# Kernel optimization log

Measured on AMD Instinct MI355X. Metric: run time of the kernel, lower is better.

Reference implementation:

```python
import jax, jax.numpy as jnp
import numpy as np

NUM_GRAPHS = 16
NODES_PER = 1024
D = 128
H = 2
KPOS = 20
E = 262144


def _ln(x, g, b):
    mu = jnp.mean(x, axis=-1, keepdims=True)
    var = jnp.mean((x - mu) ** 2, axis=-1, keepdims=True)
    return (x - mu) * jax.lax.rsqrt(var + 1e-5) * g + b


def setup_inputs() -> dict:
    key = jax.random.key(0)
    ks = jax.random.split(key, 12)
    N = NUM_GRAPHS * NODES_PER
    s = 0.02
    return {
        "x": jax.random.normal(ks[0], (N, D), jnp.float32),
        "pos_enc": jax.random.normal(ks[1], (N, KPOS), jnp.float32),
        "pe_w": jax.random.normal(ks[2], (D, KPOS), jnp.float32) * s,
        "pe_b": jnp.zeros((D,), jnp.float32),
        "in_w": jax.random.normal(ks[3], (3 * D, D), jnp.float32) * s,
        "in_b": jnp.zeros((3 * D,), jnp.float32),
        "out_w": jax.random.normal(ks[4], (D, D), jnp.float32) * s,
        "out_b": jnp.zeros((D,), jnp.float32),
        "ln1_g": jnp.ones((D,), jnp.float32),
        "ln1_b": jnp.zeros((D,), jnp.float32),
        "ln2_g": jnp.ones((D,), jnp.float32),
        "ln2_b": jnp.zeros((D,), jnp.float32),
        "ff1_w": jax.random.normal(ks[5], (4 * D, D), jnp.float32) * s,
        "ff1_b": jnp.zeros((4 * D,), jnp.float32),
        "ff2_w": jax.random.normal(ks[6], (D, 4 * D), jnp.float32) * s,
        "ff2_b": jnp.zeros((D,), jnp.float32),
        "edge_index": jax.random.randint(ks[7], (2, E), 0, N, dtype=jnp.int32),
        "batch": jnp.repeat(jnp.arange(NUM_GRAPHS, dtype=jnp.int32), NODES_PER),
    }


def reference(x, pos_enc, pe_w, pe_b, in_w, in_b, out_w, out_b,
              ln1_g, ln1_b, ln2_g, ln2_b, ff1_w, ff1_b, ff2_w, ff2_b,
              edge_index, batch):
    # pos_enc Linear + add, then per-graph transformer (graphs equal-sized -> batched)
    h = x + pos_enc @ pe_w.T + pe_b  # (N, D)
    h = h.reshape(NUM_GRAPHS, NODES_PER, D)  # (B, S, D)

    hd = D // H
    qkv = h @ in_w.T + in_b  # (B, S, 3D)
    q, k, v = jnp.split(qkv, 3, axis=-1)

    def heads(t):
        return t.reshape(NUM_GRAPHS, NODES_PER, H, hd).transpose(0, 2, 1, 3)

    q, k, v = heads(q), heads(k), heads(v)  # (B, H, S, hd)
    scores = jnp.einsum('bhqd,bhkd->bhqk', q, k) / jnp.float32(np.sqrt(hd))
    attn = jax.nn.softmax(scores, axis=-1)
    ctx = jnp.einsum('bhqk,bhkd->bhqd', attn, v)
    ctx = ctx.transpose(0, 2, 1, 3).reshape(NUM_GRAPHS, NODES_PER, D)
    sa = ctx @ out_w.T + out_b

    # post-norm (PyTorch TransformerEncoderLayer default, eval mode: no dropout)
    h = _ln(h + sa, ln1_g, ln1_b)
    ff = jax.nn.relu(h @ ff1_w.T + ff1_b) @ ff2_w.T + ff2_b
    h = _ln(h + ff, ln2_g, ln2_b)
    return h.reshape(-1, D)
```

## Files before the change

kernel.cpp:

```cpp
#include <hip/hip_runtime.h>

typedef unsigned short u16;

#define NGRAPH 16
#define SEQ    1024
#define DIM    128
#define NHEAD  2
#define HDIM   64
#define KPOS   20
#define NTOT   (NGRAPH*SEQ)
#define QKVD   (3*DIM)

__device__ __forceinline__ float bf2f(u16 u) {
    return __uint_as_float(((unsigned int)u) << 16);
}
__device__ __forceinline__ u16 f2bf(float f) {
    unsigned int u = __float_as_uint(f);
    u += 0x7fffu + ((u >> 16) & 1u);
    return (u16)(u >> 16);
}

template<int CTRL>
__device__ __forceinline__ float dpp_ror(float x) {
    return __int_as_float(__builtin_amdgcn_update_dpp(
        __float_as_int(x), __float_as_int(x), CTRL, 0xF, 0xF, true));
}
__device__ __forceinline__ float row16_max(float x) {
    x = fmaxf(x, dpp_ror<0x121>(x));
    x = fmaxf(x, dpp_ror<0x122>(x));
    x = fmaxf(x, dpp_ror<0x124>(x));
    x = fmaxf(x, dpp_ror<0x128>(x));
    return x;
}
__device__ __forceinline__ float row16_sum(float x) {
    x += dpp_ror<0x121>(x);
    x += dpp_ror<0x122>(x);
    x += dpp_ror<0x124>(x);
    x += dpp_ror<0x128>(x);
    return x;
}

__device__ __forceinline__ float ld1(const void* p, int fbf, size_t i) {
    return fbf ? bf2f(((const u16*)p)[i]) : ((const float*)p)[i];
}
__device__ __forceinline__ float4 ldw8(const void* W, int fbf, size_t i) {
    if (fbf) return *(const float4*)((const u16*)W + i);
    const float* q = (const float*)W + i;
    float4 a = *(const float4*)q, b = *(const float4*)(q + 4);
    float4 r;
    u16* d = (u16*)&r;
    d[0]=f2bf(a.x); d[1]=f2bf(a.y); d[2]=f2bf(a.z); d[3]=f2bf(a.w);
    d[4]=f2bf(b.x); d[5]=f2bf(b.y); d[6]=f2bf(b.z); d[7]=f2bf(b.w);
    return r;
}

typedef __attribute__((ext_vector_type(8))) short bf16x8;
typedef __attribute__((ext_vector_type(4))) float f32x4;

__device__ __forceinline__ void gload16(const u16* g, u16* l) {
    __builtin_amdgcn_global_load_lds(
        (const __attribute__((address_space(1))) unsigned int*)(g),
        (__attribute__((address_space(3))) unsigned int*)(l), 16, 0, 0);
}
#define VMCNT0() asm volatile("s_waitcnt vmcnt(0)" ::: "memory")

__device__ __forceinline__ int detect_bf16(const u16* x) {
    int ok = 1;
    for (int i = 0; i < 256; i += 2) {
        unsigned e = (x[i] >> 7) & 0xFF;
        if (e < 60u || e > 180u) ok = 0;
    }
    return ok;
}
__global__ void detect_kernel(const u16* __restrict__ x, int* __restrict__ flag) {
    if (threadIdx.x == 0 && blockIdx.x == 0) *flag = detect_bf16(x);
}

__global__ __launch_bounds__(256)
void wconv_kernel(const void* __restrict__ in_w, const void* __restrict__ out_w,
                  const void* __restrict__ ff1_w, const void* __restrict__ ff2_w,
                  const u16* __restrict__ x,
                  u16* __restrict__ wbf, int* __restrict__ flag) {
    __shared__ int fsh;
    if (threadIdx.x == 0) {
        int ok = detect_bf16(x);
        fsh = ok;
        if (blockIdx.x == 0) *flag = ok;
    }
    __syncthreads();
    int fbf = fsh;
    int i8 = (blockIdx.x * 256 + threadIdx.x) * 8;
    const void* src; int off;
    if      (i8 <  49152) { src = in_w;  off = i8; }
    else if (i8 <  65536) { src = out_w; off = i8 - 49152; }
    else if (i8 < 131072) { src = ff1_w; off = i8 - 65536; }
    else                  { src = ff2_w; off = i8 - 131072; }
    *(float4*)&wbf[i8] = ldw8(src, fbf, off);
}

__global__ __launch_bounds__(256)
void pe_kernel(const void* __restrict__ x, const void* __restrict__ pos,
               const void* __restrict__ pe_w, const void* __restrict__ pe_b,
               u16* __restrict__ h0, const int* __restrict__ flag) {
    int fbf = *flag;
    __shared__ float wsh[DIM][KPOS + 1];
    int t = threadIdx.x;
    for (int i = t; i < DIM * KPOS; i += 256)
        wsh[i / KPOS][i % KPOS] = ld1(pe_w, fbf, i);
    __syncthreads();
    int row = blockIdx.x * 2 + (t >> 7), d = t & 127;
    float acc = 0.f;
#pragma unroll
    for (int k = 0; k < KPOS; ++k)
        acc += ld1(pos, fbf, (size_t)row * KPOS + k) * wsh[d][k];
    int rs = fbf ? 128 : 256;
    h0[(size_t)row * rs + d] =
        f2bf(ld1(x, fbf, (size_t)row * DIM + d) + acc + ld1(pe_b, fbf, d));
}

template<int EPI, int NK>
__global__ __launch_bounds__(256)
void mgemm2_kernel(const u16* __restrict__ A, const u16* __restrict__ W,
                   const void* __restrict__ bias, const u16* __restrict__ resid,
                   const void* __restrict__ lng, const void* __restrict__ lnb,
                   void* __restrict__ outp, u16* __restrict__ vt,
                   int Mtot, int AstrIn,
                   int arow0, int orow0, const int* __restrict__ flag) {
    const int K  = NK * 128;
    const int NB = (NK > 1) ? 2 : 1;
    int fbf  = *flag;
    int rs   = fbf ? 128 : 256;
    int Astr = (AstrIn < 0) ? rs : AstrIn;
    __shared__ __align__(16) u16 Ash[NB][64][128];
    __shared__ __align__(16) u16 Wsh[NB][128][128];
    int t = threadIdx.x;
    int w = t >> 6, lane = t & 63, l16 = lane & 15, quad = lane >> 4;
    int n0 = blockIdx.x * 64;
    int m0 = blockIdx.y * 128;
    int xr = (l16 & 7) << 3;
    f32x4 acc[8] = {};

    auto stage = [&](int c, int b) {
        int kc = c * 128;
#pragma unroll
        for (int i = 0; i < 4; ++i) {
            int r = w * 4 + i * 16 + (lane >> 4);
            int s = (lane & 15) ^ (r & 7);
            gload16(&A[(size_t)(arow0 + n0 + r) * Astr + kc + s * 8],
                    &Ash[b][w * 4 + i * 16][0]);
        }
#pragma unroll
        for (int i = 0; i < 8; ++i) {
            int r = w * 4 + i * 16 + (lane >> 4);
            int s = (lane & 15) ^ (r & 7);
            gload16(&W[(size_t)(m0 + r) * K + kc + s * 8],
                    &Wsh[b][w * 4 + i * 16][0]);
        }
    };

    stage(0, 0);
#pragma unroll 1
    for (int c = 0; c < NK; ++c) {
        VMCNT0();
        __syncthreads();
        if (c + 1 < NK) stage(c + 1, (c + 1) & (NB - 1));
        int b = c & (NB - 1);
        __builtin_amdgcn_s_setprio(1);
#pragma unroll
        for (int kk = 0; kk < 4; ++kk) {
            bf16x8 af = *(const bf16x8*)&Ash[b][w * 16 + l16][(kk * 32 + quad * 8) ^ xr];
#pragma unroll
            for (int s = 0; s < 8; ++s) {
                bf16x8 bf = *(const bf16x8*)&Wsh[b][s * 16 + l16][(kk * 32 + quad * 8) ^ xr];
                acc[s] = __builtin_amdgcn_mfma_f32_16x16x32_bf16(af, bf, acc[s], 0, 0, 0);
            }
        }
        __builtin_amdgcn_s_setprio(0);
    }
    float bb[8];
#pragma unroll
    for (int s = 0; s < 8; ++s) bb[s] = ld1(bias, fbf, m0 + s * 16 + l16);
    float gg[8], be[8];
    if (EPI >= 2) {
#pragma unroll
        for (int s = 0; s < 8; ++s) {
            gg[s] = ld1(lng, fbf, s * 16 + l16);
            be[s] = ld1(lnb, fbf, s * 16 + l16);
        }
    }
#pragma unroll
    for (int r = 0; r < 4; ++r) {
        int lr = w * 16 + quad * 4 + r;
        float v[8];
#pragma unroll
        for (int s = 0; s < 8; ++s) {
            v[s] = acc[s][r] + bb[s];
            if (EPI == 1) v[s] = fmaxf(v[s], 0.f);
        }
        if (EPI <= 1) {
            if (EPI == 0 && vt != nullptr && m0 == 256) {
                int n = n0 + lr;
                int bg = n >> 10, nl = n & 1023;
#pragma unroll
                for (int s = 0; s < 8; ++s)
                    vt[((size_t)(bg * 128) + s * 16 + l16) * SEQ + nl] = f2bf(v[s]);
            } else {
                u16* o = (u16*)outp;
#pragma unroll
                for (int s = 0; s < 8; ++s)
                    o[(size_t)(n0 + lr) * Mtot + m0 + s * 16 + l16] = f2bf(v[s]);
            }
        } else {
            size_t rg = (size_t)(orow0 + n0 + lr);
#pragma unroll
            for (int s = 0; s < 8; ++s)
                v[s] += bf2f(resid[rg * rs + s * 16 + l16]);
            float sm = 0.f, sq = 0.f;
#pragma unroll
            for (int s = 0; s < 8; ++s) { sm += v[s]; sq += v[s] * v[s]; }
            sm = row16_sum(sm);
            sq = row16_sum(sq);
            float mu  = sm * (1.f / DIM);
            float var = fmaxf(sq * (1.f / DIM) - mu * mu, 0.f);
            float rsq = rsqrtf(var + 1e-5f);
            if (EPI == 2) {
                u16* o = (u16*)outp;
#pragma unroll
                for (int s = 0; s < 8; ++s)
                    o[rg * rs + s * 16 + l16] =
                        f2bf((v[s] - mu) * rsq * gg[s] + be[s]);
            } else {
                if (fbf) {
                    u16* o = (u16*)outp;
#pragma unroll
                    for (int s = 0; s < 8; ++s)
                        o[rg * 128 + s * 16 + l16] =
                            f2bf((v[s] - mu) * rsq * gg[s] + be[s]);
                } else {
                    float* o = (float*)outp;
#pragma unroll
                    for (int s = 0; s < 8; ++s)
                        o[rg * 128 + s * 16 + l16] =
                            (v[s] - mu) * rsq * gg[s] + be[s];
                }
            }
        }
    }
}

__global__ __launch_bounds__(256)
void attn2_kernel(const u16* __restrict__ qkv, const u16* __restrict__ vtp,
                  u16* __restrict__ ctx) {
    __shared__ __align__(16) u16 Qsh[64][72];
    __shared__ __align__(16) u16 Ksh[2][64][64];
    __shared__ __align__(16) u16 Vsh[2][64][64];
    __shared__ u16 Psh[64][72];
    int t    = threadIdx.x;
    int w    = t >> 6;
    int lane = t & 63;
    int l16  = lane & 15;
    int quad = lane >> 4;
    int xr   = (l16 & 7) << 3;
    int L = blockIdx.x;
    int ngh = gridDim.x >> 4;
    int qt, gh;
    if (ngh >= 8) {
        int g8 = L & 7; int rest = L >> 3;
        qt = rest & 15; gh = (rest >> 4) * 8 + g8;
    } else {
        qt = L & 15; gh = L >> 4;
    }
    int b = gh >> 1, h = gh & 1;

#pragma unroll
    for (int i = 0; i < 2; ++i) {
        int idx = t + i * 256;
        int r = idx >> 3, d8 = (idx & 7) * 8;
        size_t n = (size_t)b * SEQ + qt * 64 + r;
        float4 qv = *(const float4*)&qkv[n * QKVD + h * HDIM + d8];
        u16* qp = (u16*)&qv;
#pragma unroll
        for (int j = 0; j < 8; ++j) qp[j] = f2bf(bf2f(qp[j]) * 0.125f);
        *(float4*)&Qsh[r][d8] = qv;
    }

    const u16* kbase = qkv + (size_t)b * SEQ * QKVD + DIM + h * HDIM;
    const u16* vbase = vtp + (size_t)((b * 2 + h) * 64) * SEQ;

    auto stageKV = [&](int kt, int bf) {
#pragma unroll
        for (int i = 0; i < 2; ++i) {
            int r = w * 8 + i * 32 + (lane >> 3);
            int s = (lane & 7) ^ (r & 7);
            gload16(&kbase[(size_t)(kt * 64 + r) * QKVD + s * 8],
                    &Ksh[bf][w * 8 + i * 32][0]);
        }
#pragma unroll
        for (int i = 0; i < 2; ++i) {
            int r = w * 8 + i * 32 + (lane >> 3);
            int s = (lane & 7) ^ (r & 7);
            gload16(&vbase[(size_t)r * SEQ + kt * 64 + s * 8],
                    &Vsh[bf][w * 8 + i * 32][0]);
        }
    };

    stageKV(0, 0);
    VMCNT0();
    __syncthreads();
    bf16x8 qa0 = *(const bf16x8*)&Qsh[w * 16 + l16][quad * 8];
    bf16x8 qa1 = *(const bf16x8*)&Qsh[w * 16 + l16][32 + quad * 8];

    f32x4 o[4] = {};
    float mrow[4] = {-1e30f, -1e30f, -1e30f, -1e30f};
    float lrow[4] = {};

#pragma unroll 1
    for (int kt = 0; kt < SEQ / 64; ++kt) {
        int cur = kt & 1;
        if (kt + 1 < SEQ / 64) stageKV(kt + 1, cur ^ 1);

        float sc[4][4];
        __builtin_amdgcn_s_setprio(1);
#pragma unroll
        for (int c = 0; c < 4; ++c) {
            bf16x8 kb0 = *(const bf16x8*)&Ksh[cur][c * 16 + l16][(quad * 8) ^ xr];
            bf16x8 kb1 = *(const bf16x8*)&Ksh[cur][c * 16 + l16][(32 + quad * 8) ^ xr];
            f32x4 s = {};
            s = __builtin_amdgcn_mfma_f32_16x16x32_bf16(qa0, kb0, s, 0, 0, 0);
            s = __builtin_amdgcn_mfma_f32_16x16x32_bf16(qa1, kb1, s, 0, 0, 0);
#pragma unroll
            for (int r = 0; r < 4; ++r) sc[c][r] = s[r];
        }
        __builtin_amdgcn_s_setprio(0);
        float alpha[4];
#pragma unroll
        for (int r = 0; r < 4; ++r) {
            float mx = fmaxf(fmaxf(sc[0][r], sc[1][r]), fmaxf(sc[2][r], sc[3][r]));
            mx = row16_max(mx);
            float mnew = fmaxf(mrow[r], mx);
            alpha[r] = __expf(mrow[r] - mnew);
            mrow[r] = mnew;
            float sum = 0.f;
#pragma unroll
            for (int c = 0; c < 4; ++c) {
                float p = __expf(sc[c][r] - mnew);
                sc[c][r] = p;
                sum += p;
            }
            sum = row16_sum(sum);
            lrow[r] = lrow[r] * alpha[r] + sum;
        }
#pragma unroll
        for (int c = 0; c < 4; ++c)
#pragma unroll
            for (int r = 0; r < 4; ++r)
                Psh[w * 16 + quad * 4 + r][c * 16 + l16] = f2bf(sc[c][r]);
#pragma unroll
        for (int dt = 0; dt < 4; ++dt)
#pragma unroll
            for (int r = 0; r < 4; ++r) o[dt][r] *= alpha[r];
        bf16x8 pa0 = *(const bf16x8*)&Psh[w * 16 + l16][quad * 8];
        bf16x8 pa1 = *(const bf16x8*)&Psh[w * 16 + l16][32 + quad * 8];
        __builtin_amdgcn_s_setprio(1);
#pragma unroll
        for (int dt = 0; dt < 4; ++dt) {
            bf16x8 vb0 = *(const bf16x8*)&Vsh[cur][dt * 16 + l16][(quad * 8) ^ xr];
            bf16x8 vb1 = *(const bf16x8*)&Vsh[cur][dt * 16 + l16][(32 + quad * 8) ^ xr];
            o[dt] = __builtin_amdgcn_mfma_f32_16x16x32_bf16(pa0, vb0, o[dt], 0, 0, 0);
            o[dt] = __builtin_amdgcn_mfma_f32_16x16x32_bf16(pa1, vb1, o[dt], 0, 0, 0);
        }
        __builtin_amdgcn_s_setprio(0);
        if (kt + 1 < SEQ / 64) {
            VMCNT0();
            __syncthreads();
        }
    }
#pragma unroll
    for (int r = 0; r < 4; ++r) {
        float inv = 1.f / lrow[r];
        size_t n = (size_t)b * SEQ + qt * 64 + w * 16 + quad * 4 + r;
#pragma unroll
        for (int dt = 0; dt < 4; ++dt)
            ctx[n * DIM + h * HDIM + dt * 16 + l16] = f2bf(o[dt][r] * inv);
    }
}

template<int EPI, int NK>
__global__ __launch_bounds__(256)
void mgemm_kernel(const u16* __restrict__ A, const void* __restrict__ W,
                  int wbf16, const void* __restrict__ bias,
                  const u16* __restrict__ resid,
                  const void* __restrict__ lng, const void* __restrict__ lnb,
                  void* __restrict__ outp, u16* __restrict__ vt,
                  int Mtot, int AstrIn,
                  int arow0, int orow0, const int* __restrict__ flag) {
    const int K = NK * 128;
    int fbf  = *flag;
    int wfmt = wbf16 ? 1 : fbf;
    int rs   = fbf ? 128 : 256;
    int Astr = (AstrIn < 0) ? rs : AstrIn;
    __shared__ u16 Ash[64][136];
    __shared__ u16 Wsh[128][136];
    int t = threadIdx.x;
    int w = t >> 6, lane = t & 63, l16 = lane & 15, quad = lane >> 4;
    int n0 = blockIdx.x * 64;
    int m0 = blockIdx.y * 128;
    f32x4 acc[8] = {};
    float4 aR[4], wR[8];
#pragma unroll
    for (int i = 0; i < 4; ++i) {
        int idx = t + i * 256;
        int row = idx >> 4, k8 = (idx & 15) * 8;
        aR[i] = *(const float4*)&A[(size_t)(arow0 + n0 + row) * Astr + k8];
    }
#pragma unroll
    for (int i = 0; i < 8; ++i) {
        int idx = t + i * 256;
        int row = idx >> 4, k8 = (idx & 15) * 8;
        wR[i] = ldw8(W, wfmt, (size_t)(m0 + row) * K + k8);
    }
#pragma unroll 1
    for (int c = 0; c < NK; ++c) {
#pragma unroll
        for (int i = 0; i < 4; ++i) {
            int idx = t + i * 256;
            *(float4*)&Ash[idx >> 4][(idx & 15) * 8] = aR[i];
        }
#pragma unroll
        for (int i = 0; i < 8; ++i) {
            int idx = t + i * 256;
            *(float4*)&Wsh[idx >> 4][(idx & 15) * 8] = wR[i];
        }
        __syncthreads();
        if (c + 1 < NK) {
            int kc = (c + 1) * 128;
#pragma unroll
            for (int i = 0; i < 4; ++i) {
                int idx = t + i * 256;
                int row = idx >> 4, k8 = (idx & 15) * 8;
                aR[i] = *(const float4*)&A[(size_t)(arow0 + n0 + row) * Astr + kc + k8];
            }
#pragma unroll
            for (int i = 0; i < 8; ++i) {
                int idx = t + i * 256;
                int row = idx >> 4, k8 = (idx & 15) * 8;
                wR[i] = ldw8(W, wfmt, (size_t)(m0 + row) * K + kc + k8);
            }
        }
        __builtin_amdgcn_s_setprio(1);
#pragma unroll
        for (int kk = 0; kk < 4; ++kk) {
            bf16x8 af = *(const bf16x8*)&Ash[w * 16 + l16][kk * 32 + quad * 8];
#pragma unroll
            for (int s = 0; s < 8; ++s) {
                bf16x8 bf = *(const bf16x8*)&Wsh[s * 16 + l16][kk * 32 + quad * 8];
                acc[s] = __builtin_amdgcn_mfma_f32_16x16x32_bf16(af, bf, acc[s], 0, 0, 0);
            }
        }
        __builtin_amdgcn_s_setprio(0);
        if (c + 1 < NK) __syncthreads();
    }
    float bb[8];
#pragma unroll
    for (int s = 0; s < 8; ++s) bb[s] = ld1(bias, fbf, m0 + s * 16 + l16);
    float gg[8], be[8];
    if (EPI >= 2) {
#pragma unroll
        for (int s = 0; s < 8; ++s) {
            gg[s] = ld1(lng, fbf, s * 16 + l16);
            be[s] = ld1(lnb, fbf, s * 16 + l16);
        }
    }
#pragma unroll
    for (int r = 0; r < 4; ++r) {
        int lr = w * 16 + quad * 4 + r;
        float v[8];
#pragma unroll
        for (int s = 0; s < 8; ++s) {
            v[s] = acc[s][r] + bb[s];
            if (EPI == 1) v[s] = fmaxf(v[s], 0.f);
        }
        if (EPI <= 1) {
            u16* o = (u16*)outp;
#pragma unroll
            for (int s = 0; s < 8; ++s)
                o[(size_t)(n0 + lr) * Mtot + m0 + s * 16 + l16] = f2bf(v[s]);
        } else {
            size_t rg = (size_t)(orow0 + n0 + lr);
#pragma unroll
            for (int s = 0; s < 8; ++s)
                v[s] += bf2f(resid[rg * rs + s * 16 + l16]);
            float sm = 0.f, sq = 0.f;
#pragma unroll
            for (int s = 0; s < 8; ++s) { sm += v[s]; sq += v[s] * v[s]; }
            sm = row16_sum(sm);
            sq = row16_sum(sq);
            float mu  = sm * (1.f / DIM);
            float var = fmaxf(sq * (1.f / DIM) - mu * mu, 0.f);
            float rsq = rsqrtf(var + 1e-5f);
            if (EPI == 2) {
                u16* o = (u16*)outp;
#pragma unroll
                for (int s = 0; s < 8; ++s)
                    o[rg * rs + s * 16 + l16] =
                        f2bf((v[s] - mu) * rsq * gg[s] + be[s]);
            } else {
                if (fbf) {
                    u16* o = (u16*)outp;
#pragma unroll
                    for (int s = 0; s < 8; ++s)
                        o[rg * 128 + s * 16 + l16] =
                            f2bf((v[s] - mu) * rsq * gg[s] + be[s]);
                } else {
                    float* o = (float*)outp;
#pragma unroll
                    for (int s = 0; s < 8; ++s)
                        o[rg * 128 + s * 16 + l16] =
                            (v[s] - mu) * rsq * gg[s] + be[s];
                }
            }
        }
    }
}

__global__ __launch_bounds__(256)
void attn_lds_kernel(const u16* __restrict__ qkv, u16* __restrict__ ctx) {
    __shared__ u16 Qsh[64][72];
    __shared__ u16 Ksh[64][72];
    __shared__ u16 VshT[64][72];
    __shared__ u16 Psh[64][72];
    int t    = threadIdx.x;
    int w    = t >> 6;
    int lane = t & 63;
    int l16  = lane & 15;
    int quad = lane >> 4;
    int L = blockIdx.x;
    int qt = L & 15, gh = L >> 4;
    int b = gh >> 1, h = gh & 1;

#pragma unroll
    for (int i = 0; i < 2; ++i) {
        int idx = t + i * 256;
        int r = idx >> 3, d8 = (idx & 7) * 8;
        size_t n = (size_t)b * SEQ + qt * 64 + r;
        float4 qv = *(const float4*)&qkv[n * QKVD + h * HDIM + d8];
        u16* qp = (u16*)&qv;
#pragma unroll
        for (int j = 0; j < 8; ++j) qp[j] = f2bf(bf2f(qp[j]) * 0.125f);
        *(float4*)&Qsh[r][d8] = qv;
    }
    int kr = t >> 3, kd8 = (t & 7) * 8;
    int vr = t & 63, vdb = (t >> 6) * 16;
    float4 kR[2], vR[2];
    {
        size_t nk0 = (size_t)b * SEQ + kr;
        kR[0] = *(const float4*)&qkv[nk0 * QKVD + DIM + h * HDIM + kd8];
        kR[1] = *(const float4*)&qkv[(nk0 + 32) * QKVD + DIM + h * HDIM + kd8];
        size_t nv0 = (size_t)b * SEQ + vr;
        vR[0] = *(const float4*)&qkv[nv0 * QKVD + 2 * DIM + h * HDIM + vdb];
        vR[1] = *(const float4*)&qkv[nv0 * QKVD + 2 * DIM + h * HDIM + vdb + 8];
    }
    __syncthreads();
    bf16x8 qa0 = *(const bf16x8*)&Qsh[w * 16 + l16][quad * 8];
    bf16x8 qa1 = *(const bf16x8*)&Qsh[w * 16 + l16][32 + quad * 8];

    f32x4 o[4] = {};
    float mrow[4] = {-1e30f, -1e30f, -1e30f, -1e30f};
    float lrow[4] = {};

#pragma unroll 1
    for (int kt = 0; kt < SEQ / 64; ++kt) {
        *(float4*)&Ksh[kr][kd8]      = kR[0];
        *(float4*)&Ksh[kr + 32][kd8] = kR[1];
        {
            const u16* pa = (const u16*)&vR[0];
            const u16* pb = (const u16*)&vR[1];
#pragma unroll
            for (int j = 0; j < 8; ++j) VshT[vdb + j][vr] = pa[j];
#pragma unroll
            for (int j = 0; j < 8; ++j) VshT[vdb + 8 + j][vr] = pb[j];
        }
        __syncthreads();
        if (kt + 1 < SEQ / 64) {
            size_t nk0 = (size_t)b * SEQ + (kt + 1) * 64 + kr;
            kR[0] = *(const float4*)&qkv[nk0 * QKVD + DIM + h * HDIM + kd8];
            kR[1] = *(const float4*)&qkv[(nk0 + 32) * QKVD + DIM + h * HDIM + kd8];
            size_t nv0 = (size_t)b * SEQ + (kt + 1) * 64 + vr;
            vR[0] = *(const float4*)&qkv[nv0 * QKVD + 2 * DIM + h * HDIM + vdb];
            vR[1] = *(const float4*)&qkv[nv0 * QKVD + 2 * DIM + h * HDIM + vdb + 8];
        }
        float sc[4][4];
        __builtin_amdgcn_s_setprio(1);
#pragma unroll
        for (int c = 0; c < 4; ++c) {
            bf16x8 kb0 = *(const bf16x8*)&Ksh[c * 16 + l16][quad * 8];
            bf16x8 kb1 = *(const bf16x8*)&Ksh[c * 16 + l16][32 + quad * 8];
            f32x4 s = {};
            s = __builtin_amdgcn_mfma_f32_16x16x32_bf16(qa0, kb0, s, 0, 0, 0);
            s = __builtin_amdgcn_mfma_f32_16x16x32_bf16(qa1, kb1, s, 0, 0, 0);
#pragma unroll
            for (int r = 0; r < 4; ++r) sc[c][r] = s[r];
        }
        __builtin_amdgcn_s_setprio(0);
        float alpha[4];
#pragma unroll
        for (int r = 0; r < 4; ++r) {
            float mx = fmaxf(fmaxf(sc[0][r], sc[1][r]), fmaxf(sc[2][r], sc[3][r]));
            mx = row16_max(mx);
            float mnew = fmaxf(mrow[r], mx);
            alpha[r] = __expf(mrow[r] - mnew);
            mrow[r] = mnew;
            float sum = 0.f;
#pragma unroll
            for (int c = 0; c < 4; ++c) {
                float p = __expf(sc[c][r] - mnew);
                sc[c][r] = p;
                sum += p;
            }
            sum = row16_sum(sum);
            lrow[r] = lrow[r] * alpha[r] + sum;
        }
#pragma unroll
        for (int c = 0; c < 4; ++c)
#pragma unroll
            for (int r = 0; r < 4; ++r)
                Psh[w * 16 + quad * 4 + r][c * 16 + l16] = f2bf(sc[c][r]);
#pragma unroll
        for (int dt = 0; dt < 4; ++dt)
#pragma unroll
            for (int r = 0; r < 4; ++r) o[dt][r] *= alpha[r];
        bf16x8 pa0 = *(const bf16x8*)&Psh[w * 16 + l16][quad * 8];
        bf16x8 pa1 = *(const bf16x8*)&Psh[w * 16 + l16][32 + quad * 8];
        __builtin_amdgcn_s_setprio(1);
#pragma unroll
        for (int dt = 0; dt < 4; ++dt) {
            bf16x8 vb0 = *(const bf16x8*)&VshT[dt * 16 + l16][quad * 8];
            bf16x8 vb1 = *(const bf16x8*)&VshT[dt * 16 + l16][32 + quad * 8];
            o[dt] = __builtin_amdgcn_mfma_f32_16x16x32_bf16(pa0, vb0, o[dt], 0, 0, 0);
            o[dt] = __builtin_amdgcn_mfma_f32_16x16x32_bf16(pa1, vb1, o[dt], 0, 0, 0);
        }
        __builtin_amdgcn_s_setprio(0);
        __syncthreads();
    }
#pragma unroll
    for (int r = 0; r < 4; ++r) {
        float inv = 1.f / lrow[r];
        size_t n = (size_t)b * SEQ + qt * 64 + w * 16 + quad * 4 + r;
#pragma unroll
        for (int dt = 0; dt < 4; ++dt)
            ctx[n * DIM + h * HDIM + dt * 16 + l16] = f2bf(o[dt][r] * inv);
    }
}

extern "C" void kernel_launch(void* const* d_in, const int* in_sizes, int n_in,
                              void* d_out, int out_size, void* d_ws, size_t ws_size,
                              hipStream_t stream) {
    const void* x     = d_in[0];
    const void* pos   = d_in[1];
    const void* pe_w  = d_in[2];
    const void* pe_b  = d_in[3];
    const void* in_w  = d_in[4];
    const void* in_b  = d_in[5];
    const void* out_w = d_in[6];
    const void* out_b = d_in[7];
    const void* ln1_g = d_in[8];
    const void* ln1_b = d_in[9];
    const void* ln2_g = d_in[10];
    const void* ln2_b = d_in[11];
    const void* ff1_w = d_in[12];
    const void* ff1_b = d_in[13];
    const void* ff2_w = d_in[14];
    const void* ff2_b = d_in[15];

    char* wsb  = (char*)d_ws;
    int*  flag = (int*)(wsb + ((ws_size - 4) & ~(size_t)3));
    u16*  h01  = (u16*)d_out;
    const size_t MB = 1024 * 1024;

    if (ws_size >= 21 * MB) {
        u16* qkv = (u16*)wsb;
        u16* ctx = (u16*)(wsb + 12 * MB);
        u16* f1  = (u16*)wsb;
        u16* vt  = (u16*)(wsb + 16 * MB);
        u16* wbf = (u16*)(wsb + 20 * MB);
        u16* wb_in  = wbf;
        u16* wb_out = wbf + 49152;
        u16* wb_ff1 = wbf + 65536;
        u16* wb_ff2 = wbf + 131072;

        wconv_kernel<<<96, 256, 0, stream>>>(in_w, out_w, ff1_w, ff2_w,
                                             (const u16*)x, wbf, flag);
        pe_kernel<<<NTOT / 2, 256, 0, stream>>>(x, pos, pe_w, pe_b, h01, flag);
        mgemm2_kernel<0,1><<<dim3(NTOT / 64, 3), 256, 0, stream>>>(
            h01, wb_in, in_b, nullptr, nullptr, nullptr, qkv, vt,
            QKVD, -1, 0, 0, flag);
        attn2_kernel<<<NGRAPH * NHEAD * 16, 256, 0, stream>>>(qkv, vt, ctx);
        mgemm2_kernel<2,1><<<dim3(NTOT / 64, 1), 256, 0, stream>>>(
            ctx, wb_out, out_b, h01, ln1_g, ln1_b, h01, nullptr,
            DIM, DIM, 0, 0, flag);
        mgemm2_kernel<1,1><<<dim3(NTOT / 64, 4), 256, 0, stream>>>(
            h01, wb_ff1, ff1_b, nullptr, nullptr, nullptr, f1, nullptr,
            4 * DIM, -1, 0, 0, flag);
        mgemm2_kernel<3,4><<<dim3(NTOT / 64, 1), 256, 0, stream>>>(
            f1, wb_ff2, ff2_b, h01, ln2_g, ln2_b, d_out, nullptr,
            DIM, 4 * DIM, 0, 0, flag);
    } else {
        u16* qkv_g = (u16*)wsb;
        u16* ctx_g = (u16*)(wsb + 768 * 1024);
        u16* f1_g  = (u16*)wsb;
        detect_kernel<<<1, 1, 0, stream>>>((const u16*)x, flag);
        pe_kernel<<<NTOT / 2, 256, 0, stream>>>(x, pos, pe_w, pe_b, h01, flag);
        for (int g = 0; g < NGRAPH; ++g) {
            int row0 = g * SEQ;
            mgemm_kernel<0,1><<<dim3(SEQ / 64, 3), 256, 0, stream>>>(
                h01, in_w, 0, in_b, nullptr, nullptr, nullptr, qkv_g, nullptr,
                QKVD, -1, row0, 0, flag);
            attn_lds_kernel<<<NHEAD * 16, 256, 0, stream>>>(qkv_g, ctx_g);
            mgemm_kernel<2,1><<<dim3(SEQ / 64, 1), 256, 0, stream>>>(
                ctx_g, out_w, 0, out_b, h01, ln1_g, ln1_b, h01, nullptr,
                DIM, DIM, 0, row0, flag);
        }
        for (int g = 0; g < NGRAPH; ++g) {
            int row0 = g * SEQ;
            mgemm_kernel<1,1><<<dim3(SEQ / 64, 4), 256, 0, stream>>>(
                h01, ff1_w, 0, ff1_b, nullptr, nullptr, nullptr, f1_g, nullptr,
                4 * DIM, -1, row0, 0, flag);
            mgemm_kernel<3,4><<<dim3(SEQ / 64, 1), 256, 0, stream>>>(
                f1_g, ff2_w, 0, ff2_b, h01, ln2_g, ln2_b, d_out, nullptr,
                DIM, 4 * DIM, 0, row0, flag);
        }
    }
}
```

Measured before the change: 187.7 us.

## Loop over output column tiles per block to reuse A tile in QKV and FF1 GEMMs

Adds a GEMM kernel where each block loads its 64-row activation tile once and iterates over all 128-column weight tiles. Weight tiles are double-buffered in LDS so the next one is prefetched while the current one is computed. This replaces the 2D grid that reloaded the same A tile for every output column tile in the QKV and FF1 projections. The cost is fewer blocks (256 instead of 768 or 1024) and a more serialized per-block loop, which can lower occupancy and latency hiding.

```diff
diff --git a/kernel.cpp b/kernel.cpp
--- a/kernel.cpp
+++ b/kernel.cpp
@@ -116,6 +116,94 @@
     int rs = fbf ? 128 : 256;
     h0[(size_t)row * rs + d] =
         f2bf(ld1(x, fbf, (size_t)row * DIM + d) + acc + ld1(pe_b, fbf, d));
+}
+
+template<int EPI, int MREP>
+__global__ __launch_bounds__(256)
+void mgemmM_kernel(const u16* __restrict__ A, const u16* __restrict__ W,
+                   const void* __restrict__ bias, void* __restrict__ outp,
+                   u16* __restrict__ vt, int Mtot, int AstrIn,
+                   const int* __restrict__ flag) {
+    int fbf  = *flag;
+    int rs   = fbf ? 128 : 256;
+    int Astr = (AstrIn < 0) ? rs : AstrIn;
+    __shared__ __align__(16) u16 Ash[64][128];
+    __shared__ __align__(16) u16 Wsh[2][128][128];
+    int t = threadIdx.x;
+    int w = t >> 6, lane = t & 63, l16 = lane & 15, quad = lane >> 4;
+    int n0 = blockIdx.x * 64;
+    int xr = (l16 & 7) << 3;
+
+#pragma unroll
+    for (int i = 0; i < 4; ++i) {
+        int r = w * 4 + i * 16 + (lane >> 4);
+        int s = (lane & 15) ^ (r & 7);
+        gload16(&A[(size_t)(n0 + r) * Astr + s * 8], &Ash[w * 4 + i * 16][0]);
+    }
+#pragma unroll
+    for (int i = 0; i < 8; ++i) {
+        int r = w * 4 + i * 16 + (lane >> 4);
+        int s = (lane & 15) ^ (r & 7);
+        gload16(&W[(size_t)r * 128 + s * 8], &Wsh[0][w * 4 + i * 16][0]);
+    }
+
+#pragma unroll
+    for (int m = 0; m < MREP; ++m) {
+        int m0 = m * 128;
+        if (m + 1 < MREP) {
+#pragma unroll
+            for (int i = 0; i < 8; ++i) {
+                int r = w * 4 + i * 16 + (lane >> 4);
+                int s = (lane & 15) ^ (r & 7);
+                gload16(&W[(size_t)(m0 + 128 + r) * 128 + s * 8],
+                        &Wsh[(m + 1) & 1][w * 4 + i * 16][0]);
+            }
+            asm volatile("s_waitcnt vmcnt(8)" ::: "memory");
+        } else {
+            asm volatile("s_waitcnt vmcnt(0)" ::: "memory");
+        }
+        __builtin_amdgcn_s_barrier();
+
+        f32x4 acc[8] = {};
+        __builtin_amdgcn_s_setprio(1);
+#pragma unroll
+        for (int kk = 0; kk < 4; ++kk) {
+            bf16x8 af = *(const bf16x8*)&Ash[w * 16 + l16][(kk * 32 + quad * 8) ^ xr];
+#pragma unroll
+            for (int s = 0; s < 8; ++s) {
+                bf16x8 bf = *(const bf16x8*)&Wsh[m & 1][s * 16 + l16][(kk * 32 + quad * 8) ^ xr];
+                acc[s] = __builtin_amdgcn_mfma_f32_16x16x32_bf16(af, bf, acc[s], 0, 0, 0);
+            }
+        }
+        __builtin_amdgcn_s_setprio(0);
+
+        float bb[8];
+#pragma unroll
+        for (int s = 0; s < 8; ++s) bb[s] = ld1(bias, fbf, m0 + s * 16 + l16);
+#pragma unroll
+        for (int r = 0; r < 4; ++r) {
+            int lr = w * 16 + quad * 4 + r;
+            float v[8];
+#pragma unroll
+            for (int s = 0; s < 8; ++s) {
+                v[s] = acc[s][r] + bb[s];
+                if (EPI == 1) v[s] = fmaxf(v[s], 0.f);
+            }
+            if (EPI == 0 && MREP == 3 && m == 2 && vt != nullptr) {
+                int n = n0 + lr;
+                int bg = n >> 10, nl = n & 1023;
+#pragma unroll
+                for (int s = 0; s < 8; ++s)
+                    vt[((size_t)(bg * 128) + s * 16 + l16) * SEQ + nl] = f2bf(v[s]);
+            } else {
+                u16* o = (u16*)outp;
+#pragma unroll
+                for (int s = 0; s < 8; ++s)
+                    o[(size_t)(n0 + lr) * Mtot + m0 + s * 16 + l16] = f2bf(v[s]);
+            }
+        }
+        if (m + 1 < MREP) __builtin_amdgcn_s_barrier();
+    }
 }
 
 template<int EPI, int NK>
@@ -691,16 +779,14 @@
         wconv_kernel<<<96, 256, 0, stream>>>(in_w, out_w, ff1_w, ff2_w,
                                              (const u16*)x, wbf, flag);
         pe_kernel<<<NTOT / 2, 256, 0, stream>>>(x, pos, pe_w, pe_b, h01, flag);
-        mgemm2_kernel<0,1><<<dim3(NTOT / 64, 3), 256, 0, stream>>>(
-            h01, wb_in, in_b, nullptr, nullptr, nullptr, qkv, vt,
-            QKVD, -1, 0, 0, flag);
+        mgemmM_kernel<0,3><<<NTOT / 64, 256, 0, stream>>>(
+            h01, wb_in, in_b, qkv, vt, QKVD, -1, flag);
         attn2_kernel<<<NGRAPH * NHEAD * 16, 256, 0, stream>>>(qkv, vt, ctx);
         mgemm2_kernel<2,1><<<dim3(NTOT / 64, 1), 256, 0, stream>>>(
             ctx, wb_out, out_b, h01, ln1_g, ln1_b, h01, nullptr,
             DIM, DIM, 0, 0, flag);
-        mgemm2_kernel<1,1><<<dim3(NTOT / 64, 4), 256, 0, stream>>>(
-            h01, wb_ff1, ff1_b, nullptr, nullptr, nullptr, f1, nullptr,
-            4 * DIM, -1, 0, 0, flag);
+        mgemmM_kernel<1,4><<<NTOT / 64, 256, 0, stream>>>(
+            h01, wb_ff1, ff1_b, f1, nullptr, 4 * DIM, -1, flag);
         mgemm2_kernel<3,4><<<dim3(NTOT / 64, 1), 256, 0, stream>>>(
             f1, wb_ff2, ff2_b, h01, ln2_g, ln2_b, d_out, nullptr,
             DIM, 4 * DIM, 0, 0, flag);
```

Measured after the change: 189.1 us. No clear change (+0.8%).
